# Kernel tuning notes

Measured on AMD Instinct MI355X. Metric: run time of the kernel, lower is better.

The kernel has to match this reference:

```python
import jax, jax.numpy as jnp
import numpy as np

N_HEAD = 4
N_FEAT = 256
D_K = N_FEAT // N_HEAD
MAX_SEQ_LEN = 500
LN_EPS = 1e-6


def setup_inputs() -> dict:
    key = jax.random.key(0)
    ks = jax.random.split(key, 12)
    B, L, F = 64, 500, N_FEAT
    s = lambda fan_in: 1.0 / np.sqrt(fan_in)
    return {
        "q": jax.random.normal(ks[0], (B, L, F), jnp.float32),
        "k": jax.random.normal(ks[1], (B, L, F), jnp.float32),
        "v": jax.random.normal(ks[2], (B, L, F), jnp.float32),
        # weights stored as [in, out] (torch Linear transposed)
        "w_qs": jax.random.normal(ks[3], (F, F), jnp.float32) * s(F),
        "w_vs": jax.random.normal(ks[4], (F, F), jnp.float32) * s(F),
        "w1": jax.random.normal(ks[5], (D_K, D_K), jnp.float32) * s(D_K),
        "b1": jax.random.normal(ks[6], (D_K,), jnp.float32) * s(D_K),
        "w2": jax.random.normal(ks[7], (D_K, MAX_SEQ_LEN), jnp.float32) * s(D_K),
        "b2": jax.random.normal(ks[8], (MAX_SEQ_LEN,), jnp.float32) * s(D_K),
        "fc_w": jax.random.normal(ks[9], (F, F), jnp.float32) * s(F),
        "ln_g": jnp.ones((F,), jnp.float32),
        "ln_b": jnp.zeros((F,), jnp.float32),
    }


def reference(q, k, v, w_qs, w_vs, w1, b1, w2, b2, fc_w, ln_g, ln_b):
    B, L, F = q.shape
    H, dk = N_HEAD, D_K
    residual = q
    # head projections -> [B, H, L, dk]
    qh = (q @ w_qs).reshape(B, L, H, dk).transpose(0, 2, 1, 3)
    vh = (v @ w_vs).reshape(B, L, H, dk).transpose(0, 2, 1, 3)
    # dense synthesizer: relu(q W1 + b1) W2 + b2, slice to len_q
    weight = jax.nn.relu(qh @ w1 + b1)
    attn = (weight @ w2 + b2)[..., :L]            # [B, H, L, L]
    attn = jax.nn.softmax(attn, axis=-1)
    out = attn @ vh                                # [B, H, L, dk]
    out = out.transpose(0, 2, 1, 3).reshape(B, L, F)
    out = out @ fc_w + residual
    # LayerNorm(eps=1e-6)
    mu = jnp.mean(out, axis=-1, keepdims=True)
    var = jnp.var(out, axis=-1, keepdims=True)
    out = (out - mu) * jax.lax.rsqrt(var + LN_EPS) * ln_g + ln_b
    return out
```

## Files before the change

kernel.cpp:

```cpp
#include <hip/hip_runtime.h>
#include <math.h>

#define B_   64
#define L_   500
#define F_   256
#define H_   4
#define DK   64
#define LOG2E 1.44269504088896340736f

typedef unsigned short u16;
typedef unsigned int   u32;
typedef __attribute__((ext_vector_type(8))) short short8;
typedef __attribute__((ext_vector_type(4))) float f32x4;

static __device__ __forceinline__ u16 f2bf(float f) {
    u32 u = __float_as_uint(f);
    u32 r = (u + 0x7FFFu + ((u >> 16) & 1u)) >> 16;
    return (u16)r;
}
static __device__ __forceinline__ u32 pk_bf16_up(float x, float y) {
    u32 xb = __float_as_uint(x) + 0x8000u;
    u32 yb = __float_as_uint(y) + 0x8000u;
    return (xb >> 16) | (yb & 0xFFFF0000u);
}
static __device__ __forceinline__ float exp2_fast(float x) {
#if __has_builtin(__builtin_amdgcn_exp2f)
    return __builtin_amdgcn_exp2f(x);
#else
    return exp2f(x);
#endif
}

typedef __attribute__((address_space(3))) u32 lds32;
typedef const __attribute__((address_space(1))) u32 gbl32;
static __device__ __forceinline__ void gload_lds16(const u16* g, u16* l) {
    __builtin_amdgcn_global_load_lds((gbl32*)g, (lds32*)l, 16, 0, 0);
}

__global__ __launch_bounds__(256) void prep_kernel(
    const float* __restrict__ wq, const float* __restrict__ wv,
    const float* __restrict__ fcw, const float* __restrict__ w1,
    const float* __restrict__ w2, const float* __restrict__ b2,
    u16* __restrict__ wqsw, u16* __restrict__ wvsw, u16* __restrict__ fcwT,
    u16* __restrict__ w1T, u16* __restrict__ w2sw,
    u16* __restrict__ qh_bf, u16* __restrict__ vhT, float* __restrict__ b2p)
{
    int t = blockIdx.x * 256 + threadIdx.x;
    int stride = gridDim.x * 256;
    for (int i = t; i < 256 * 256; i += stride) {
        int n = i >> 8, k = i & 255;
        fcwT[i] = f2bf(fcw[k * 256 + n]);
    }
    for (int i = t; i < 256 * 256; i += stride) {
        int kc = i >> 14;
        int n  = (i >> 6) & 255;
        int k  = i & 63;
        int kl = kc * 64 + (k ^ ((n & 7) << 3));
        wqsw[i] = f2bf(wq[kl * 256 + n]);
        wvsw[i] = f2bf(wv[kl * 256 + n]);
    }
    for (int i = t; i < 64 * 64; i += stride) {
        int n = i >> 6, k = i & 63;
        w1T[i] = f2bf(w1[k * 64 + n]);
    }
    for (int i = t; i < 512 * 64; i += stride) {
        int cc  = i >> 12;
        int row = (i >> 6) & 63;
        int kc  = i & 63;
        int n   = cc * 64 + row;
        int kl  = kc ^ ((row & 7) << 3);
        w2sw[i] = f2bf((n < 500 ? w2[kl * 500 + n] : 0.f) * LOG2E);
    }
    for (int i = t; i < 512; i += stride)
        b2p[i] = (i < 500) ? b2[i] * LOG2E : -1e30f;
    for (int i = t; i < 3072; i += stride)
        qh_bf[8192000 + i] = 0;
    for (int i = t; i < 196608; i += stride) {
        int bh = i / 768;
        int r  = i - bh * 768;
        int d  = r / 12;
        int kk = 52 + (r - d * 12);
        vhT[((size_t)((bh * 8 + 7) * 64 + d)) * 64 + (kk ^ ((d & 7) << 3))] = 0;
    }
}

__global__ __launch_bounds__(512, 1) void proj_kernel(
    const float* __restrict__ q, const float* __restrict__ v,
    const u16* __restrict__ wqsw, const u16* __restrict__ wvsw,
    u16* __restrict__ qh_bf, u16* __restrict__ vhT)
{
    const int which = blockIdx.y;
    const float* __restrict__ x = which ? v : q;
    const u16*   __restrict__ wsw = which ? wvsw : wqsw;

    __shared__ __align__(16) u16 Xs[128 * 256];
    __shared__ __align__(16) u16 Ws[2][16384];

    const int tid  = threadIdx.x;
    const int wvid = tid >> 6, ln = tid & 63;
    const int n16  = ln & 15, quad = ln >> 4;
    const int wr   = wvid >> 2, wc = wvid & 3;
    const int row0 = blockIdx.x * 128;

    float4 xv[16];
    #pragma unroll
    for (int j = 0; j < 16; j++) {
        int idx = tid + 512 * j;
        int m = idx >> 6, k4 = idx & 63;
        xv[j] = *(const float4*)&x[(size_t)(row0 + m) * 256 + k4 * 4];
    }
    #pragma unroll
    for (int j = 0; j < 4; j++)
        gload_lds16(wsw + wvid * 2048 + j * 512 + ln * 8,
                    &Ws[0][wvid * 2048 + j * 512]);
    #pragma unroll
    for (int j = 0; j < 16; j++) {
        int idx = tid + 512 * j;
        int m = idx >> 6, k = (idx & 63) * 4;
        int kx = k ^ ((m & 7) << 3);
        *(uint2*)&Xs[m * 256 + kx] =
            make_uint2(pk_bf16_up(xv[j].x, xv[j].y), pk_bf16_up(xv[j].z, xv[j].w));
    }

    f32x4 acc[4][4];
    #pragma unroll
    for (int mt = 0; mt < 4; mt++)
        #pragma unroll
        for (int nt = 0; nt < 4; nt++) acc[mt][nt] = (f32x4){0.f, 0.f, 0.f, 0.f};

    __syncthreads();

    #pragma unroll 2
    for (int cc = 0; cc < 4; cc++) {
        if (cc < 3) {
            #pragma unroll
            for (int j = 0; j < 4; j++)
                gload_lds16(wsw + (cc + 1) * 16384 + wvid * 2048 + j * 512 + ln * 8,
                            &Ws[(cc + 1) & 1][wvid * 2048 + j * 512]);
        }
        const u16* wb = &Ws[cc & 1][0];
        #pragma unroll
        for (int ks = 0; ks < 2; ks++) {
            short8 af[4], bfr[4];
            #pragma unroll
            for (int mt = 0; mt < 4; mt++) {
                int m = wr * 64 + mt * 16 + n16;
                int k = cc * 64 + ks * 32 + quad * 8;
                af[mt] = *(const short8*)&Xs[m * 256 + (k ^ ((m & 7) << 3))];
            }
            #pragma unroll
            for (int nt = 0; nt < 4; nt++) {
                int r = wc * 64 + nt * 16 + n16;
                bfr[nt] = *(const short8*)&wb[r * 64 +
                                              ((ks * 32 + quad * 8) ^ ((r & 7) << 3))];
            }
            #pragma unroll
            for (int mt = 0; mt < 4; mt++)
                #pragma unroll
                for (int nt = 0; nt < 4; nt++)
                    acc[mt][nt] = __builtin_amdgcn_mfma_f32_16x16x32_bf16(
                        af[mt], bfr[nt], acc[mt][nt], 0, 0, 0);
        }
        __syncthreads();
    }

    if (which == 0) {
        #pragma unroll
        for (int mt = 0; mt < 4; mt++) {
            int m0 = row0 + wr * 64 + mt * 16 + quad * 4;
            int b  = m0 / 500;
            int l0 = m0 - 500 * b;
            #pragma unroll
            for (int nt = 0; nt < 4; nt++) {
                int d = nt * 16 + n16;
                u16* dst = qh_bf + ((size_t)((b * 4 + wc) * 500 + l0)) * 64 + d;
                #pragma unroll
                for (int i = 0; i < 4; i++)
                    dst[(size_t)i * 64] = f2bf(acc[mt][nt][i]);
            }
        }
    } else {
        #pragma unroll
        for (int mt = 0; mt < 4; mt++) {
            int m0 = row0 + wr * 64 + mt * 16 + quad * 4;
            int b  = m0 / 500;
            int l0 = m0 - 500 * b;
            int vc = l0 >> 6, kk = l0 & 63;
            #pragma unroll
            for (int nt = 0; nt < 4; nt++) {
                int d = nt * 16 + n16;
                __align__(8) u16 t4[4];
                #pragma unroll
                for (int i = 0; i < 4; i++) t4[i] = f2bf(acc[mt][nt][i]);
                size_t base = ((size_t)(((b * 4 + wc) * 8 + vc) * 64 + d)) * 64;
                *(uint2*)&vhT[base + (kk ^ ((d & 7) << 3))] = *(const uint2*)t4;
            }
        }
    }
}

__global__ __launch_bounds__(512, 1) void attn_kernel(
    const u16* __restrict__ qh, const u16* __restrict__ vhT,
    const u16* __restrict__ w1T, const float* __restrict__ b1,
    const u16* __restrict__ w2sw, const float* __restrict__ b2p,
    u16* __restrict__ ctx)
{
    __shared__ __align__(16) u16 w2all[32768];
    __shared__ __align__(16) u16 v_s[2][4096];
    __shared__ __align__(16) float b2s[512];
    __shared__ __align__(16) u16 scr[8][4][16][72];

    const int tid  = threadIdx.x;
    const int wv   = tid >> 6;
    const int ln   = tid & 63;
    const int n16  = ln & 15;
    const int quad = ln >> 4;
    const int bh   = blockIdx.x;
    const int r0   = wv * 64;

    const u16* vg = vhT + (size_t)bh * 32768;

    {
        int base = wv * 4096;
        #pragma unroll
        for (int j = 0; j < 8; j++)
            gload_lds16(w2sw + base + j * 512 + ln * 8, &w2all[base + j * 512]);
        gload_lds16(vg + wv * 512 + ln * 8, &v_s[0][wv * 512]);
        if (wv < 2)
            gload_lds16((const u16*)b2p + wv * 512 + ln * 8, (u16*)&b2s[wv * 256]);
    }

    const int b = bh >> 2, h = bh & 3;

    {
        short8 a0[4], a1[4];
        #pragma unroll
        for (int rg = 0; rg < 4; rg++) {
            const u16* qbase =
                qh + ((size_t)(bh * 500 + r0 + rg * 16 + n16)) * 64;
            a0[rg] = *(const short8*)(qbase + quad * 8);
            a1[rg] = *(const short8*)(qbase + 32 + quad * 8);
        }
        #pragma unroll
        for (int nt = 0; nt < 4; nt++) {
            const u16* wb = w1T + (nt * 16 + n16) * 64;
            short8 wA0 = *(const short8*)(wb + quad * 8);
            short8 wA1 = *(const short8*)(wb + 32 + quad * 8);
            float4 bv = *(const float4*)&b1[nt * 16 + quad * 4];
            #pragma unroll
            for (int rg = 0; rg < 4; rg++) {
                f32x4 c = {bv.x, bv.y, bv.z, bv.w};
                c = __builtin_amdgcn_mfma_f32_16x16x32_bf16(wA0, a0[rg], c, 0, 0, 0);
                c = __builtin_amdgcn_mfma_f32_16x16x32_bf16(wA1, a1[rg], c, 0, 0, 0);
                u32 p01 = pk_bf16_up(fmaxf(c[0], 0.f), fmaxf(c[1], 0.f));
                u32 p23 = pk_bf16_up(fmaxf(c[2], 0.f), fmaxf(c[3], 0.f));
                *(uint2*)&scr[wv][rg][n16][nt * 16 + quad * 4] =
                    make_uint2(p01, p23);
            }
        }
    }
    short8 sa0[4], sa1[4];
    #pragma unroll
    for (int rg = 0; rg < 4; rg++) {
        sa0[rg] = *(const short8*)&scr[wv][rg][n16][quad * 8];
        sa1[rg] = *(const short8*)&scr[wv][rg][n16][32 + quad * 8];
    }

    f32x4 oacc[4][4];
    #pragma unroll
    for (int rg = 0; rg < 4; rg++)
        #pragma unroll
        for (int nt = 0; nt < 4; nt++)
            oacc[rg][nt] = (f32x4){0.f, 0.f, 0.f, 0.f};
    float sm[4] = {0.f, 0.f, 0.f, 0.f};

    __syncthreads();

    #pragma unroll 2
    for (int cc = 0; cc < 8; cc++) {
        if (cc < 7)
            gload_lds16(vg + (cc + 1) * 4096 + wv * 512 + ln * 8,
                        &v_s[(cc + 1) & 1][wv * 512]);
        const u16* vbuf = &v_s[cc & 1][0];

        #pragma unroll
        for (int t = 0; t < 4; t++) {
            int r  = t * 16 + n16;
            int sw = (r & 7) << 3;
            const u16* wb = &w2all[cc * 4096 + r * 64];
            short8 wA0 = *(const short8*)&wb[(quad * 8) ^ sw];
            short8 wA1 = *(const short8*)&wb[(32 + quad * 8) ^ sw];
            float4 bv = *(const float4*)&b2s[cc * 64 + t * 16 + quad * 4];
            #pragma unroll
            for (int rg = 0; rg < 4; rg++) {
                f32x4 c = {bv.x, bv.y, bv.z, bv.w};
                c = __builtin_amdgcn_mfma_f32_16x16x32_bf16(wA0, sa0[rg], c, 0, 0, 0);
                c = __builtin_amdgcn_mfma_f32_16x16x32_bf16(wA1, sa1[rg], c, 0, 0, 0);
                float e0 = exp2_fast(c[0]);
                float e1 = exp2_fast(c[1]);
                float e2 = exp2_fast(c[2]);
                float e3 = exp2_fast(c[3]);
                sm[rg] += (e0 + e1) + (e2 + e3);
                *(uint2*)&scr[wv][rg][n16][t * 16 + quad * 4] =
                    make_uint2(pk_bf16_up(e0, e1), pk_bf16_up(e2, e3));
            }
        }
        #pragma unroll
        for (int ks = 0; ks < 2; ks++) {
            short8 pa[4];
            #pragma unroll
            for (int rg = 0; rg < 4; rg++)
                pa[rg] = *(const short8*)&scr[wv][rg][n16][ks * 32 + quad * 8];
            #pragma unroll
            for (int nt = 0; nt < 4; nt++) {
                int d   = nt * 16 + n16;
                int swd = (d & 7) << 3;
                short8 vb = *(const short8*)&vbuf[d * 64 +
                                                  ((ks * 32 + quad * 8) ^ swd)];
                #pragma unroll
                for (int rg = 0; rg < 4; rg++)
                    oacc[rg][nt] = __builtin_amdgcn_mfma_f32_16x16x32_bf16(
                        pa[rg], vb, oacc[rg][nt], 0, 0, 0);
            }
        }
        __syncthreads();
    }

    #pragma unroll
    for (int rg = 0; rg < 4; rg++) {
        float smt = sm[rg];
        smt += __shfl_xor(smt, 16);
        smt += __shfl_xor(smt, 32);
        #pragma unroll
        for (int i = 0; i < 4; i++) {
            int lrow = r0 + rg * 16 + quad * 4 + i;
            float si = __shfl(smt, quad * 4 + i);
            if (lrow < 500) {
                float s = 1.f / si;
                u16* dst = &ctx[((size_t)(b * 500 + lrow)) * 256 + h * 64];
                #pragma unroll
                for (int nt = 0; nt < 4; nt++)
                    dst[nt * 16 + n16] = f2bf(oacc[rg][nt][i] * s);
            }
        }
    }
}

__global__ __launch_bounds__(512) void final_kernel(
    const u16* __restrict__ ctx, const u16* __restrict__ fcwT,
    const float* __restrict__ qres, const float* __restrict__ g,
    const float* __restrict__ bta, float* __restrict__ out)
{
    __shared__ u16 Xs[64][72];
    __shared__ u16 Ws[256][72];
    __shared__ float red[4][2][64];
    __shared__ float murs[2][64];

    const int tid  = threadIdx.x;
    const int wvid = tid >> 6, ln = tid & 63;
    const int n16  = ln & 15, quad = ln >> 4;
    const int wr   = wvid >> 2, wc = wvid & 3;
    const int row0 = blockIdx.x * 64;

    f32x4 acc[2][4];
    #pragma unroll
    for (int mt = 0; mt < 2; mt++)
        #pragma unroll
        for (int nt = 0; nt < 4; nt++) acc[mt][nt] = (f32x4){0.f, 0.f, 0.f, 0.f};

    for (int kc = 0; kc < 256; kc += 64) {
        {
            int idx = tid;
            int m = idx >> 3, k8 = idx & 7;
            *(uint4*)&Xs[m][k8 * 8] =
                *(const uint4*)&ctx[(size_t)(row0 + m) * 256 + kc + k8 * 8];
        }
        #pragma unroll
        for (int j = 0; j < 4; j++) {
            int idx = tid + 512 * j;
            int n = idx >> 3, k8 = idx & 7;
            *(uint4*)&Ws[n][k8 * 8] = *(const uint4*)&fcwT[n * 256 + kc + k8 * 8];
        }
        __syncthreads();
        #pragma unroll
        for (int ks = 0; ks < 2; ks++) {
            short8 af[2], bfr[4];
            #pragma unroll
            for (int mt = 0; mt < 2; mt++)
                af[mt] = *(const short8*)&Xs[wr * 32 + mt * 16 + n16][ks * 32 + quad * 8];
            #pragma unroll
            for (int nt = 0; nt < 4; nt++)
                bfr[nt] = *(const short8*)&Ws[wc * 64 + nt * 16 + n16][ks * 32 + quad * 8];
            #pragma unroll
            for (int mt = 0; mt < 2; mt++)
                #pragma unroll
                for (int nt = 0; nt < 4; nt++)
                    acc[mt][nt] = __builtin_amdgcn_mfma_f32_16x16x32_bf16(
                        af[mt], bfr[nt], acc[mt][nt], 0, 0, 0);
        }
        __syncthreads();
    }

    #pragma unroll
    for (int mt = 0; mt < 2; mt++) {
        int m0 = row0 + wr * 32 + mt * 16 + quad * 4;
        #pragma unroll
        for (int i = 0; i < 4; i++) {
            const float* rp = &qres[(size_t)(m0 + i) * 256 + wc * 64 + n16];
            #pragma unroll
            for (int nt = 0; nt < 4; nt++)
                acc[mt][nt][i] += rp[nt * 16];
        }
    }
    #pragma unroll
    for (int mt = 0; mt < 2; mt++) {
        #pragma unroll
        for (int i = 0; i < 4; i++) {
            float s1 = 0.f, s2 = 0.f;
            #pragma unroll
            for (int nt = 0; nt < 4; nt++) {
                float vv = acc[mt][nt][i];
                s1 += vv; s2 += vv * vv;
            }
            #pragma unroll
            for (int off = 1; off < 16; off <<= 1) {
                s1 += __shfl_xor(s1, off);
                s2 += __shfl_xor(s2, off);
            }
            if (n16 == 0) {
                int r = wr * 32 + mt * 16 + quad * 4 + i;
                red[wc][0][r] = s1;
                red[wc][1][r] = s2;
            }
        }
    }
    __syncthreads();
    if (tid < 64) {
        float S1 = red[0][0][tid] + red[1][0][tid] + red[2][0][tid] + red[3][0][tid];
        float S2 = red[0][1][tid] + red[1][1][tid] + red[2][1][tid] + red[3][1][tid];
        float mu  = S1 * 0.00390625f;
        float var = S2 * 0.00390625f - mu * mu;
        murs[0][tid] = mu;
        murs[1][tid] = rsqrtf(var + 1e-6f);
    }
    __syncthreads();

    float gv[4], bv[4];
    #pragma unroll
    for (int nt = 0; nt < 4; nt++) {
        int col = wc * 64 + nt * 16 + n16;
        gv[nt] = g[col];
        bv[nt] = bta[col];
    }
    #pragma unroll
    for (int mt = 0; mt < 2; mt++) {
        int rb = wr * 32 + mt * 16 + quad * 4;
        #pragma unroll
        for (int i = 0; i < 4; i++) {
            float mu = murs[0][rb + i];
            float rs = murs[1][rb + i];
            float* op = &out[(size_t)(row0 + rb + i) * 256 + wc * 64 + n16];
            #pragma unroll
            for (int nt = 0; nt < 4; nt++)
                op[nt * 16] = (acc[mt][nt][i] - mu) * rs * gv[nt] + bv[nt];
        }
    }
}

extern "C" void kernel_launch(void* const* d_in, const int* in_sizes, int n_in,
                              void* d_out, int out_size, void* d_ws, size_t ws_size,
                              hipStream_t stream)
{
    const float* q   = (const float*)d_in[0];
    const float* v   = (const float*)d_in[2];
    const float* wqs = (const float*)d_in[3];
    const float* wvs = (const float*)d_in[4];
    const float* w1  = (const float*)d_in[5];
    const float* b1  = (const float*)d_in[6];
    const float* w2  = (const float*)d_in[7];
    const float* b2  = (const float*)d_in[8];
    const float* fcw = (const float*)d_in[9];
    const float* lng = (const float*)d_in[10];
    const float* lnb = (const float*)d_in[11];
    float* out = (float*)d_out;

    u16* qh_bf = (u16*)d_ws;
    u16* vhT   = qh_bf + 8200192;
    u16* w1T   = vhT + 8388608;
    u16* w2sw  = w1T + 4096;
    u16* wqsw  = w2sw + 32768;
    u16* wvsw  = wqsw + 65536;
    u16* fcwT  = wvsw + 65536;
    u16* ctx   = fcwT + 65536;
    float* b2p = (float*)(qh_bf + 8195072);

    prep_kernel <<<dim3(64),     256, 0, stream>>>(wqs, wvs, fcw, w1, w2, b2,
                                                   wqsw, wvsw, fcwT, w1T, w2sw,
                                                   qh_bf, vhT, b2p);
    proj_kernel <<<dim3(250, 2), 512, 0, stream>>>(q, v, wqsw, wvsw, qh_bf, vhT);
    attn_kernel <<<dim3(256),    512, 0, stream>>>(qh_bf, vhT, w1T, b1, w2sw, b2p, ctx);
    final_kernel<<<dim3(500),    512, 0, stream>>>(ctx, fcwT, q, lng, lnb, out);
}
```

Measured before the change: 89.60 us.

## Keep full projection weight resident in LDS and stream X fragments from global

The projection kernel now loads the whole 256x256 bf16 weight into LDS once per block and loops over four 64-row chunks, halving the grid to 125x2 blocks. The X tile is no longer staged through LDS; each lane loads its A-fragment straight from global fp32 memory and converts it to bf16 in registers. This removes the per-chunk weight double-buffering, the barriers and the X staging, and amortizes the weight load over more rows. The cost is uncoalesced, latency-exposed global loads for X inside the MFMA loop and a large LDS footprint.

```diff
diff --git a/kernel.cpp b/kernel.cpp
--- a/kernel.cpp
+++ b/kernel.cpp
@@ -93,107 +93,93 @@
     const float* __restrict__ x = which ? v : q;
     const u16*   __restrict__ wsw = which ? wvsw : wqsw;
 
-    __shared__ __align__(16) u16 Xs[128 * 256];
-    __shared__ __align__(16) u16 Ws[2][16384];
+    __shared__ __align__(16) u16 Wlds[65536];
 
     const int tid  = threadIdx.x;
     const int wvid = tid >> 6, ln = tid & 63;
     const int n16  = ln & 15, quad = ln >> 4;
     const int wr   = wvid >> 2, wc = wvid & 3;
-    const int row0 = blockIdx.x * 128;
-
-    float4 xv[16];
-    #pragma unroll
-    for (int j = 0; j < 16; j++) {
-        int idx = tid + 512 * j;
-        int m = idx >> 6, k4 = idx & 63;
-        xv[j] = *(const float4*)&x[(size_t)(row0 + m) * 256 + k4 * 4];
-    }
-    #pragma unroll
-    for (int j = 0; j < 4; j++)
-        gload_lds16(wsw + wvid * 2048 + j * 512 + ln * 8,
-                    &Ws[0][wvid * 2048 + j * 512]);
-    #pragma unroll
-    for (int j = 0; j < 16; j++) {
-        int idx = tid + 512 * j;
-        int m = idx >> 6, k = (idx & 63) * 4;
-        int kx = k ^ ((m & 7) << 3);
-        *(uint2*)&Xs[m * 256 + kx] =
-            make_uint2(pk_bf16_up(xv[j].x, xv[j].y), pk_bf16_up(xv[j].z, xv[j].w));
-    }
-
-    f32x4 acc[4][4];
-    #pragma unroll
-    for (int mt = 0; mt < 4; mt++)
-        #pragma unroll
-        for (int nt = 0; nt < 4; nt++) acc[mt][nt] = (f32x4){0.f, 0.f, 0.f, 0.f};
-
+    const int base0 = blockIdx.x * 256;
+
+    {
+        int base = wvid * 8192;
+        #pragma unroll
+        for (int j = 0; j < 16; j++)
+            gload_lds16(wsw + base + j * 512 + ln * 8, &Wlds[base + j * 512]);
+    }
     __syncthreads();
 
-    #pragma unroll 2
-    for (int cc = 0; cc < 4; cc++) {
-        if (cc < 3) {
-            #pragma unroll
-            for (int j = 0; j < 4; j++)
-                gload_lds16(wsw + (cc + 1) * 16384 + wvid * 2048 + j * 512 + ln * 8,
-                            &Ws[(cc + 1) & 1][wvid * 2048 + j * 512]);
-        }
-        const u16* wb = &Ws[cc & 1][0];
-        #pragma unroll
-        for (int ks = 0; ks < 2; ks++) {
-            short8 af[4], bfr[4];
-            #pragma unroll
-            for (int mt = 0; mt < 4; mt++) {
-                int m = wr * 64 + mt * 16 + n16;
-                int k = cc * 64 + ks * 32 + quad * 8;
-                af[mt] = *(const short8*)&Xs[m * 256 + (k ^ ((m & 7) << 3))];
+    #pragma unroll 1
+    for (int rc = 0; rc < 4; rc++) {
+        const int r0 = base0 + rc * 64;
+
+        f32x4 acc[2][4];
+        #pragma unroll
+        for (int mt = 0; mt < 2; mt++)
+            #pragma unroll
+            for (int nt = 0; nt < 4; nt++) acc[mt][nt] = (f32x4){0.f, 0.f, 0.f, 0.f};
+
+        #pragma unroll
+        for (int kq = 0; kq < 8; kq++) {
+            const int kc = kq >> 1, ks = kq & 1;
+            const int kk = kq * 32 + quad * 8;
+            short8 af[2];
+            #pragma unroll
+            for (int mt = 0; mt < 2; mt++) {
+                int m = r0 + wr * 32 + mt * 16 + n16;
+                const float* xp = &x[(size_t)m * 256 + kk];
+                float4 xa = *(const float4*)xp;
+                float4 xb = *(const float4*)(xp + 4);
+                union { short8 s; u32 u[4]; } tconv;
+                tconv.u[0] = pk_bf16_up(xa.x, xa.y);
+                tconv.u[1] = pk_bf16_up(xa.z, xa.w);
+                tconv.u[2] = pk_bf16_up(xb.x, xb.y);
+                tconv.u[3] = pk_bf16_up(xb.z, xb.w);
+                af[mt] = tconv.s;
             }
             #pragma unroll
             for (int nt = 0; nt < 4; nt++) {
                 int r = wc * 64 + nt * 16 + n16;
-                bfr[nt] = *(const short8*)&wb[r * 64 +
-                                              ((ks * 32 + quad * 8) ^ ((r & 7) << 3))];
-            }
-            #pragma unroll
-            for (int mt = 0; mt < 4; mt++)
-                #pragma unroll
-                for (int nt = 0; nt < 4; nt++)
+                short8 bfr = *(const short8*)&Wlds[kc * 16384 + r * 64 +
+                                 (((ks * 32) + quad * 8) ^ ((r & 7) << 3))];
+                #pragma unroll
+                for (int mt = 0; mt < 2; mt++)
                     acc[mt][nt] = __builtin_amdgcn_mfma_f32_16x16x32_bf16(
-                        af[mt], bfr[nt], acc[mt][nt], 0, 0, 0);
-        }
-        __syncthreads();
-    }
-
-    if (which == 0) {
-        #pragma unroll
-        for (int mt = 0; mt < 4; mt++) {
-            int m0 = row0 + wr * 64 + mt * 16 + quad * 4;
-            int b  = m0 / 500;
-            int l0 = m0 - 500 * b;
-            #pragma unroll
-            for (int nt = 0; nt < 4; nt++) {
-                int d = nt * 16 + n16;
-                u16* dst = qh_bf + ((size_t)((b * 4 + wc) * 500 + l0)) * 64 + d;
-                #pragma unroll
-                for (int i = 0; i < 4; i++)
-                    dst[(size_t)i * 64] = f2bf(acc[mt][nt][i]);
-            }
-        }
-    } else {
-        #pragma unroll
-        for (int mt = 0; mt < 4; mt++) {
-            int m0 = row0 + wr * 64 + mt * 16 + quad * 4;
-            int b  = m0 / 500;
-            int l0 = m0 - 500 * b;
-            int vc = l0 >> 6, kk = l0 & 63;
-            #pragma unroll
-            for (int nt = 0; nt < 4; nt++) {
-                int d = nt * 16 + n16;
-                __align__(8) u16 t4[4];
-                #pragma unroll
-                for (int i = 0; i < 4; i++) t4[i] = f2bf(acc[mt][nt][i]);
-                size_t base = ((size_t)(((b * 4 + wc) * 8 + vc) * 64 + d)) * 64;
-                *(uint2*)&vhT[base + (kk ^ ((d & 7) << 3))] = *(const uint2*)t4;
+                        af[mt], bfr, acc[mt][nt], 0, 0, 0);
+            }
+        }
+
+        if (which == 0) {
+            #pragma unroll
+            for (int mt = 0; mt < 2; mt++) {
+                int m0 = r0 + wr * 32 + mt * 16 + quad * 4;
+                int b  = m0 / 500;
+                int l0 = m0 - 500 * b;
+                #pragma unroll
+                for (int nt = 0; nt < 4; nt++) {
+                    int d = nt * 16 + n16;
+                    u16* dst = qh_bf + ((size_t)((b * 4 + wc) * 500 + l0)) * 64 + d;
+                    #pragma unroll
+                    for (int i = 0; i < 4; i++)
+                        dst[(size_t)i * 64] = f2bf(acc[mt][nt][i]);
+                }
+            }
+        } else {
+            #pragma unroll
+            for (int mt = 0; mt < 2; mt++) {
+                int m0 = r0 + wr * 32 + mt * 16 + quad * 4;
+                int b  = m0 / 500;
+                int l0 = m0 - 500 * b;
+                int vc = l0 >> 6, kk2 = l0 & 63;
+                #pragma unroll
+                for (int nt = 0; nt < 4; nt++) {
+                    int d = nt * 16 + n16;
+                    __align__(8) u16 t4[4];
+                    #pragma unroll
+                    for (int i = 0; i < 4; i++) t4[i] = f2bf(acc[mt][nt][i]);
+                    size_t base = ((size_t)(((b * 4 + wc) * 8 + vc) * 64 + d)) * 64;
+                    *(uint2*)&vhT[base + (kk2 ^ ((d & 7) << 3))] = *(const uint2*)t4;
+                }
             }
         }
     }
@@ -497,7 +483,7 @@
     prep_kernel <<<dim3(64),     256, 0, stream>>>(wqs, wvs, fcw, w1, w2, b2,
                                                    wqsw, wvsw, fcwT, w1T, w2sw,
                                                    qh_bf, vhT, b2p);
-    proj_kernel <<<dim3(250, 2), 512, 0, stream>>>(q, v, wqsw, wvsw, qh_bf, vhT);
+    proj_kernel <<<dim3(125, 2), 512, 0, stream>>>(q, v, wqsw, wvsw, qh_bf, vhT);
     attn_kernel <<<dim3(256),    512, 0, stream>>>(qh_bf, vhT, w1T, b1, w2sw, b2p, ctx);
     final_kernel<<<dim3(500),    512, 0, stream>>>(ctx, fcwT, q, lng, lnb, out);
 }
```

New measurement: 98.39 us. 1.1x slower.
